# Kernel optimization log

Hardware: AMD Instinct MI355X
Metric: run time of the kernel (lower is better)

The kernel has to match this reference:

```python
import jax, jax.numpy as jnp
import numpy as np

MARGIN = 0.3  # hard-coded in all three MarginRankingLoss instances


def setup_inputs() -> dict:
    key = jax.random.key(0)
    k1, k2, k3, k4 = jax.random.split(key, 4)
    n, d, num_ids = 4096, 2048, 100
    inputs = jax.random.normal(k1, (n, d), dtype=jnp.float32)
    targets_a = jax.random.randint(k2, (n,), 0, num_ids, dtype=jnp.int64)
    targets_b = jax.random.randint(k3, (n,), 0, num_ids, dtype=jnp.int64)
    lam = jax.random.uniform(k4, (), dtype=jnp.float32)
    epoch = 60
    return {"inputs": inputs, "targets_a": targets_a, "targets_b": targets_b,
            "lam": lam, "epoch": epoch}


def reference(inputs, targets_a, targets_b, lam, epoch):
    # pairwise euclidean distance: dist[i,j] = ||x_i - x_j||
    sq = jnp.sum(inputs * inputs, axis=1)                      # [n]
    dist = sq[:, None] + sq[None, :] - 2.0 * (inputs @ inputs.T)
    dist = jnp.sqrt(jnp.clip(dist, 1e-12))                     # [n, n]

    ma = targets_a[:, None] == targets_a[None, :]
    mb = targets_b[:, None] == targets_b[None, :]
    m_same_ab = ma & mb                                        # same a AND b (incl. diagonal)
    m_same_or = (ma & ~mb) | (~ma & mb)                        # exactly one of a/b matches
    m_dif_ab = ~ma & ~mb                                       # neither matches

    ninf = -jnp.inf
    pinf = jnp.inf
    hp = jnp.max(jnp.where(m_same_ab, dist, ninf), axis=1)     # hardest positive
    hn = jnp.min(jnp.where(m_dif_ab, dist, pinf), axis=1)      # hardest negative
    max_or = jnp.max(jnp.where(m_same_or, dist, ninf), axis=1)
    min_or = jnp.min(jnp.where(m_same_or, dist, pinf), axis=1)

    use_or = m_same_or.any(axis=1) & (epoch > 50)
    sp = jnp.where(use_or, max_or, hp)
    sn = jnp.where(use_or, min_or, hn)

    # MarginRankingLoss(x1, x2, y=1) = mean(relu(x2 - x1 + margin))
    loss_1 = jnp.mean(jnp.maximum(0.0, hp - hn + MARGIN))
    loss_2 = jnp.mean(jnp.maximum(0.0, sp - hn + MARGIN))
    loss_3 = jnp.mean(jnp.maximum(0.0, hp - sn + MARGIN))
    return loss_1 + loss_2 + loss_3
```

## Files before the change

### kernel.cpp

```cpp
#include <hip/hip_runtime.h>
#include <hip/hip_bf16.h>

#define NROW 4096
#define KDIM 2048
#define ROWB (KDIM * 2)
#define BT 256
#define BK 64
#define NT (KDIM / BK)
#define LDSBUF 65536
#define PHI(r) (((r) & 7) << 4)

typedef __attribute__((ext_vector_type(8))) short bf16x8;
typedef __attribute__((ext_vector_type(4))) float f32x4;
typedef __attribute__((ext_vector_type(4))) unsigned short u16x4;

__device__ __forceinline__ unsigned short f2bf(float x) {
    unsigned u = __float_as_uint(x);
    unsigned r = (u + 0x7FFFu + ((u >> 16) & 1u)) >> 16;
    return (unsigned short)r;
}
__device__ __forceinline__ float bf2f(unsigned short b) {
    return __uint_as_float(((unsigned)b) << 16);
}

__global__ __launch_bounds__(256) void k_convert(const float* __restrict__ X,
                                                 unsigned short* __restrict__ Xb,
                                                 float* __restrict__ sqv) {
    const int row = blockIdx.x;
    const int t = threadIdx.x;
    const float4* xr = (const float4*)(X + (size_t)row * KDIM);
    unsigned short* br = Xb + (size_t)row * KDIM;
    float acc = 0.f;
#pragma unroll
    for (int it = 0; it < 2; ++it) {
        int idx = t * 2 + it;
        float4 v = xr[idx];
        u16x4 b;
        b.x = f2bf(v.x); b.y = f2bf(v.y); b.z = f2bf(v.z); b.w = f2bf(v.w);
        float f0 = bf2f(b.x), f1 = bf2f(b.y), f2 = bf2f(b.z), f3 = bf2f(b.w);
        acc += f0 * f0 + f1 * f1 + f2 * f2 + f3 * f3;
        *(u16x4*)(br + idx * 4) = b;
    }
#pragma unroll
    for (int s = 32; s > 0; s >>= 1) acc += __shfl_xor(acc, s);
    __shared__ float red[4];
    const int lane = t & 63, wid = t >> 6;
    if (lane == 0) red[wid] = acc;
    __syncthreads();
    if (t == 0) sqv[row] = red[0] + red[1] + red[2] + red[3];
}

__global__ __launch_bounds__(256) void k_init(unsigned* hp, unsigned* hn,
                                              unsigned* mor, unsigned* mir,
                                              int* anyor, float* out) {
    int i = blockIdx.x * 256 + threadIdx.x;
    hp[i] = 0u;
    hn[i] = 0x7F800000u;
    mor[i] = 0u;
    mir[i] = 0x7F800000u;
    anyor[i] = 0;
    if (i == 0) out[0] = 0.f;
}

__global__ __launch_bounds__(512, 2) void k_gemm(const unsigned short* __restrict__ Xb,
                                                 const float* __restrict__ sqv,
                                                 const int* __restrict__ ta,
                                                 const int* __restrict__ tb,
                                                 unsigned int* __restrict__ hp,
                                                 unsigned int* __restrict__ hn,
                                                 unsigned int* __restrict__ mor,
                                                 unsigned int* __restrict__ mir,
                                                 int* __restrict__ anyor) {
    __shared__ char lds[2 * LDSBUF];
    const int bi = blockIdx.x >> 4;
    const int bj = blockIdx.x & 15;
    const int t = threadIdx.x;
    const int lane = t & 63;
    const int w = t >> 6;
    const int wm = w >> 2;
    const int wn = w & 3;
    const int l15 = lane & 15;
    const int kg16 = (lane >> 4) * 16;
    const char* xbase = (const char*)Xb;

    int aoff[8][2], boff[4][2];
#pragma unroll
    for (int m = 0; m < 8; ++m) {
        const int r = wm * 128 + m * 16 + l15;
#pragma unroll
        for (int ks = 0; ks < 2; ++ks)
            aoff[m][ks] = r * 128 + ((ks * 64 + kg16) ^ PHI(r));
    }
#pragma unroll
    for (int n = 0; n < 4; ++n) {
        const int j = wn * 64 + n * 16 + l15;
#pragma unroll
        for (int ks = 0; ks < 2; ++ks)
            boff[n][ks] = 32768 + j * 128 + ((ks * 64 + kg16) ^ PHI(j));
    }

    f32x4 acc[8][4] = {};

#define STAGE(tt, p)                                                          \
    do {                                                                      \
        constexpr int isb_ = (p) >= 4;                                        \
        constexpr int c_ = (p) - isb_ * 4;                                    \
        const int row_ = c_ * 64 + (t >> 3);                                  \
        const int gr_ = (isb_ ? bj : bi) * BT + row_;                         \
        const char* gsrc_ = xbase + (size_t)gr_ * ROWB + (size_t)(tt) * 128 + \
                            (((t & 7) * 16) ^ PHI(row_));                     \
        char* ldst_ = lds + ((tt) & 1) * LDSBUF + isb_ * 32768 + row_ * 128 + \
                      (t & 7) * 16;                                           \
        __builtin_amdgcn_global_load_lds(                                     \
            (const __attribute__((address_space(1))) void*)gsrc_,             \
            (__attribute__((address_space(3))) void*)ldst_, 16, 0, 0);        \
    } while (0)

    STAGE(0, 0); STAGE(0, 2); STAGE(0, 4); STAGE(0, 5);
    STAGE(0, 6); STAGE(0, 7); STAGE(0, 1); STAGE(0, 3);
    asm volatile("s_waitcnt vmcnt(2)" ::: "memory");
    __builtin_amdgcn_s_barrier();

    bf16x8 af[4][2], bfr[4][2];
    for (int tk = 0; tk < NT; ++tk) {
        const char* bufb = lds + (tk & 1) * LDSBUF;
        const bool stg = (tk + 1) < NT;

        if (stg) { STAGE(tk + 1, 0); STAGE(tk + 1, 2); STAGE(tk + 1, 4); STAGE(tk + 1, 5); }
#pragma unroll
        for (int m = 0; m < 4; ++m) {
            af[m][0] = *(const bf16x8*)(bufb + aoff[m][0]);
            af[m][1] = *(const bf16x8*)(bufb + aoff[m][1]);
        }
#pragma unroll
        for (int n = 0; n < 2; ++n) {
            bfr[n][0] = *(const bf16x8*)(bufb + boff[n][0]);
            bfr[n][1] = *(const bf16x8*)(bufb + boff[n][1]);
        }
        __builtin_amdgcn_s_barrier();
        __builtin_amdgcn_s_setprio(1);
#pragma unroll
        for (int ks = 0; ks < 2; ++ks)
#pragma unroll
            for (int m = 0; m < 4; ++m) {
                acc[m][0] = __builtin_amdgcn_mfma_f32_16x16x32_bf16(af[m][ks], bfr[0][ks], acc[m][0], 0, 0, 0);
                acc[m][1] = __builtin_amdgcn_mfma_f32_16x16x32_bf16(af[m][ks], bfr[1][ks], acc[m][1], 0, 0, 0);
            }
        __builtin_amdgcn_s_setprio(0);
        __builtin_amdgcn_s_barrier();

        if (stg) { STAGE(tk + 1, 6); STAGE(tk + 1, 7); STAGE(tk + 1, 1); STAGE(tk + 1, 3); }
#pragma unroll
        for (int n = 2; n < 4; ++n) {
            bfr[n][0] = *(const bf16x8*)(bufb + boff[n][0]);
            bfr[n][1] = *(const bf16x8*)(bufb + boff[n][1]);
        }
        __builtin_amdgcn_s_barrier();
        __builtin_amdgcn_s_setprio(1);
#pragma unroll
        for (int ks = 0; ks < 2; ++ks)
#pragma unroll
            for (int m = 0; m < 4; ++m) {
                acc[m][2] = __builtin_amdgcn_mfma_f32_16x16x32_bf16(af[m][ks], bfr[2][ks], acc[m][2], 0, 0, 0);
                acc[m][3] = __builtin_amdgcn_mfma_f32_16x16x32_bf16(af[m][ks], bfr[3][ks], acc[m][3], 0, 0, 0);
            }
        __builtin_amdgcn_s_setprio(0);
        if (stg)
            asm volatile("s_waitcnt vmcnt(8)" ::: "memory");
        else
            asm volatile("s_waitcnt vmcnt(0)" ::: "memory");
        __builtin_amdgcn_s_barrier();

#pragma unroll
        for (int m = 0; m < 4; ++m) {
            af[m][0] = *(const bf16x8*)(bufb + aoff[4 + m][0]);
            af[m][1] = *(const bf16x8*)(bufb + aoff[4 + m][1]);
        }
        __builtin_amdgcn_s_barrier();
        __builtin_amdgcn_s_setprio(1);
#pragma unroll
        for (int ks = 0; ks < 2; ++ks)
#pragma unroll
            for (int m = 0; m < 4; ++m) {
                acc[4 + m][2] = __builtin_amdgcn_mfma_f32_16x16x32_bf16(af[m][ks], bfr[2][ks], acc[4 + m][2], 0, 0, 0);
                acc[4 + m][3] = __builtin_amdgcn_mfma_f32_16x16x32_bf16(af[m][ks], bfr[3][ks], acc[4 + m][3], 0, 0, 0);
            }
        __builtin_amdgcn_s_setprio(0);
        __builtin_amdgcn_s_barrier();

        __builtin_amdgcn_s_setprio(1);
#pragma unroll
        for (int ks = 0; ks < 2; ++ks)
#pragma unroll
            for (int m = 0; m < 4; ++m) {
                acc[4 + m][0] = __builtin_amdgcn_mfma_f32_16x16x32_bf16(af[m][ks], bfr[0][ks], acc[4 + m][0], 0, 0, 0);
                acc[4 + m][1] = __builtin_amdgcn_mfma_f32_16x16x32_bf16(af[m][ks], bfr[1][ks], acc[4 + m][1], 0, 0, 0);
            }
        __builtin_amdgcn_s_setprio(0);
        if (stg) asm volatile("s_waitcnt vmcnt(2)" ::: "memory");
        __builtin_amdgcn_s_barrier();
    }
#undef STAGE

    float sqj[4];
    int taj[4], tbj[4];
#pragma unroll
    for (int n = 0; n < 4; ++n) {
        int j = bj * BT + wn * 64 + n * 16 + l15;
        sqj[n] = sqv[j];
        taj[n] = ta[j];
        tbj[n] = tb[j];
    }
    const float INF = __uint_as_float(0x7F800000u);
#pragma unroll
    for (int m = 0; m < 8; ++m) {
#pragma unroll
        for (int reg = 0; reg < 4; ++reg) {
            const int i = bi * BT + wm * 128 + m * 16 + (lane >> 4) * 4 + reg;
            const float sqi = sqv[i];
            const int tai = ta[i], tbi = tb[i];
            float vhp = 0.f, vhn = INF, vmor = 0.f, vmir = INF, vany = 0.f;
#pragma unroll
            for (int n = 0; n < 4; ++n) {
                float d2 = sqi + sqj[n] - 2.f * acc[m][n][reg];
                float d = sqrtf(fmaxf(d2, 1e-12f));
                bool ma = (tai == taj[n]), mb = (tbi == tbj[n]);
                if (ma && mb) {
                    vhp = fmaxf(vhp, d);
                } else if (ma != mb) {
                    vmor = fmaxf(vmor, d);
                    vmir = fminf(vmir, d);
                    vany = 1.f;
                } else {
                    vhn = fminf(vhn, d);
                }
            }
#pragma unroll
            for (int s = 1; s < 16; s <<= 1) {
                vhp = fmaxf(vhp, __shfl_xor(vhp, s, 16));
                vhn = fminf(vhn, __shfl_xor(vhn, s, 16));
                vmor = fmaxf(vmor, __shfl_xor(vmor, s, 16));
                vmir = fminf(vmir, __shfl_xor(vmir, s, 16));
                vany = fmaxf(vany, __shfl_xor(vany, s, 16));
            }
            if (l15 == 0) {
                if (vhp > 0.f) atomicMax(&hp[i], __float_as_uint(vhp));
                if (vhn < INF) atomicMin(&hn[i], __float_as_uint(vhn));
                if (vany > 0.f) {
                    atomicMax(&mor[i], __float_as_uint(vmor));
                    atomicMin(&mir[i], __float_as_uint(vmir));
                    atomicOr(&anyor[i], 1);
                }
            }
        }
    }
}

__global__ __launch_bounds__(256) void k_final(const unsigned* __restrict__ hp,
                                               const unsigned* __restrict__ hn,
                                               const unsigned* __restrict__ mor,
                                               const unsigned* __restrict__ mir,
                                               const int* __restrict__ anyor,
                                               const int* __restrict__ epoch_p,
                                               float* __restrict__ out) {
    const int t = threadIdx.x;
    const int i = blockIdx.x * 256 + t;
    const bool eok = (*epoch_p > 50);
    float fhp = __uint_as_float(hp[i]);
    float fhn = __uint_as_float(hn[i]);
    bool use_or = (anyor[i] != 0) && eok;
    float sp = use_or ? __uint_as_float(mor[i]) : fhp;
    float sn = use_or ? __uint_as_float(mir[i]) : fhn;
    float s = fmaxf(0.f, fhp - fhn + 0.3f) + fmaxf(0.f, sp - fhn + 0.3f) +
              fmaxf(0.f, fhp - sn + 0.3f);
#pragma unroll
    for (int sh = 32; sh > 0; sh >>= 1) s += __shfl_xor(s, sh);
    __shared__ float red[4];
    const int lane = t & 63, wid = t >> 6;
    if (lane == 0) red[wid] = s;
    __syncthreads();
    if (t == 0)
        atomicAdd(out, (red[0] + red[1] + red[2] + red[3]) * (1.f / 4096.f));
}

extern "C" void kernel_launch(void* const* d_in, const int* in_sizes, int n_in,
                              void* d_out, int out_size, void* d_ws, size_t ws_size,
                              hipStream_t stream) {
    const float* X = (const float*)d_in[0];
    const int* ta = (const int*)d_in[1];
    const int* tb = (const int*)d_in[2];
    const int* epoch_p = (const int*)d_in[4];
    float* out = (float*)d_out;

    char* ws = (char*)d_ws;
    unsigned short* Xb = (unsigned short*)ws;
    size_t off = (size_t)NROW * KDIM * sizeof(unsigned short);
    float* sqv = (float*)(ws + off); off += (size_t)NROW * 4;
    unsigned* hp = (unsigned*)(ws + off); off += (size_t)NROW * 4;
    unsigned* hn = (unsigned*)(ws + off); off += (size_t)NROW * 4;
    unsigned* mor = (unsigned*)(ws + off); off += (size_t)NROW * 4;
    unsigned* mir = (unsigned*)(ws + off); off += (size_t)NROW * 4;
    int* anyor = (int*)(ws + off); off += (size_t)NROW * 4;

    k_convert<<<NROW, 256, 0, stream>>>(X, Xb, sqv);
    k_init<<<NROW / 256, 256, 0, stream>>>(hp, hn, mor, mir, anyor, out);
    k_gemm<<<(NROW / BT) * (NROW / BT), 512, 0, stream>>>(Xb, sqv, ta, tb,
                                                          hp, hn, mor, mir, anyor);
    k_final<<<NROW / 256, 256, 0, stream>>>(hp, hn, mor, mir, anyor, epoch_p, out);
}
```

Before: 109.6 us.

## Prefetch next tile's A/B fragments across iterations and cut barriers in GEMM loop

Restructures the main MFMA loop so the first A fragments and B01 fragments for the next k-tile are loaded from the other LDS buffer at the end of the current iteration, using separate register sets (af0/af1, b01/b23). It reorders the global-to-LDS staging so more loads are issued up front, and drops several block barriers per iteration. It also replaces the per-fragment offset arrays with two base offsets plus constant strides to free registers. The goal is to overlap LDS reads with MFMA work and reduce sync stalls, at the cost of more live fragment registers and tighter correctness constraints on the waitcnt and barrier placement for buffer reuse.

Result: no change. 108.2 us (-1.3%).

```diff
diff --git a/kernel.cpp b/kernel.cpp
--- a/kernel.cpp
+++ b/kernel.cpp
@@ -13,6 +13,8 @@
 typedef __attribute__((ext_vector_type(8))) short bf16x8;
 typedef __attribute__((ext_vector_type(4))) float f32x4;
 typedef __attribute__((ext_vector_type(4))) unsigned short u16x4;
+
+#define MFMA16(a, b, c) __builtin_amdgcn_mfma_f32_16x16x32_bf16((a), (b), (c), 0, 0, 0)
 
 __device__ __forceinline__ unsigned short f2bf(float x) {
     unsigned u = __float_as_uint(x);
@@ -83,20 +85,13 @@
     const int kg16 = (lane >> 4) * 16;
     const char* xbase = (const char*)Xb;
 
-    int aoff[8][2], boff[4][2];
-#pragma unroll
-    for (int m = 0; m < 8; ++m) {
-        const int r = wm * 128 + m * 16 + l15;
-#pragma unroll
-        for (int ks = 0; ks < 2; ++ks)
-            aoff[m][ks] = r * 128 + ((ks * 64 + kg16) ^ PHI(r));
-    }
-#pragma unroll
-    for (int n = 0; n < 4; ++n) {
-        const int j = wn * 64 + n * 16 + l15;
-#pragma unroll
-        for (int ks = 0; ks < 2; ++ks)
-            boff[n][ks] = 32768 + j * 128 + ((ks * 64 + kg16) ^ PHI(j));
+    const int P = (l15 & 7) << 4;
+    int akb[2], bkb[2];
+#pragma unroll
+    for (int ks = 0; ks < 2; ++ks) {
+        const int kx = (ks * 64 + kg16) ^ P;
+        akb[ks] = (wm * 128 + l15) * 128 + kx;
+        bkb[ks] = 32768 + (wn * 64 + l15) * 128 + kx;
     }
 
     f32x4 acc[8][4] = {};
@@ -121,83 +116,97 @@
     asm volatile("s_waitcnt vmcnt(2)" ::: "memory");
     __builtin_amdgcn_s_barrier();
 
-    bf16x8 af[4][2], bfr[4][2];
+    bf16x8 af0[4][2], af1[4][2], b01[2][2], b23[2][2];
+#pragma unroll
+    for (int ks = 0; ks < 2; ++ks) {
+#pragma unroll
+        for (int m = 0; m < 4; ++m)
+            af0[m][ks] = *(const bf16x8*)(lds + akb[ks] + m * 2048);
+        b01[0][ks] = *(const bf16x8*)(lds + bkb[ks]);
+        b01[1][ks] = *(const bf16x8*)(lds + bkb[ks] + 2048);
+    }
+
     for (int tk = 0; tk < NT; ++tk) {
-        const char* bufb = lds + (tk & 1) * LDSBUF;
+        const char* bufc = lds + (tk & 1) * LDSBUF;
+        const char* bufn = lds + ((tk + 1) & 1) * LDSBUF;
         const bool stg = (tk + 1) < NT;
 
-        if (stg) { STAGE(tk + 1, 0); STAGE(tk + 1, 2); STAGE(tk + 1, 4); STAGE(tk + 1, 5); }
-#pragma unroll
-        for (int m = 0; m < 4; ++m) {
-            af[m][0] = *(const bf16x8*)(bufb + aoff[m][0]);
-            af[m][1] = *(const bf16x8*)(bufb + aoff[m][1]);
-        }
-#pragma unroll
-        for (int n = 0; n < 2; ++n) {
-            bfr[n][0] = *(const bf16x8*)(bufb + boff[n][0]);
-            bfr[n][1] = *(const bf16x8*)(bufb + boff[n][1]);
+        if (stg) {
+            STAGE(tk + 1, 0); STAGE(tk + 1, 2); STAGE(tk + 1, 4);
+            STAGE(tk + 1, 5); STAGE(tk + 1, 6); STAGE(tk + 1, 7);
+        }
+#pragma unroll
+        for (int ks = 0; ks < 2; ++ks) {
+            b23[0][ks] = *(const bf16x8*)(bufc + bkb[ks] + 2 * 2048);
+            b23[1][ks] = *(const bf16x8*)(bufc + bkb[ks] + 3 * 2048);
+        }
+        __builtin_amdgcn_s_setprio(1);
+#pragma unroll
+        for (int ks = 0; ks < 2; ++ks)
+#pragma unroll
+            for (int m = 0; m < 4; ++m) {
+                acc[m][0] = MFMA16(af0[m][ks], b01[0][ks], acc[m][0]);
+                acc[m][1] = MFMA16(af0[m][ks], b01[1][ks], acc[m][1]);
+            }
+        __builtin_amdgcn_s_setprio(0);
+
+        if (stg) {
+            STAGE(tk + 1, 1); STAGE(tk + 1, 3);
+            asm volatile("s_waitcnt vmcnt(8)" ::: "memory");
+        } else {
+            asm volatile("s_waitcnt vmcnt(0)" ::: "memory");
         }
         __builtin_amdgcn_s_barrier();
+#pragma unroll
+        for (int ks = 0; ks < 2; ++ks)
+#pragma unroll
+            for (int m = 0; m < 4; ++m)
+                af1[m][ks] = *(const bf16x8*)(bufc + akb[ks] + (4 + m) * 2048);
         __builtin_amdgcn_s_setprio(1);
 #pragma unroll
         for (int ks = 0; ks < 2; ++ks)
 #pragma unroll
             for (int m = 0; m < 4; ++m) {
-                acc[m][0] = __builtin_amdgcn_mfma_f32_16x16x32_bf16(af[m][ks], bfr[0][ks], acc[m][0], 0, 0, 0);
-                acc[m][1] = __builtin_amdgcn_mfma_f32_16x16x32_bf16(af[m][ks], bfr[1][ks], acc[m][1], 0, 0, 0);
+                acc[m][2] = MFMA16(af0[m][ks], b23[0][ks], acc[m][2]);
+                acc[m][3] = MFMA16(af0[m][ks], b23[1][ks], acc[m][3]);
             }
         __builtin_amdgcn_s_setprio(0);
-        __builtin_amdgcn_s_barrier();
-
-        if (stg) { STAGE(tk + 1, 6); STAGE(tk + 1, 7); STAGE(tk + 1, 1); STAGE(tk + 1, 3); }
-#pragma unroll
-        for (int n = 2; n < 4; ++n) {
-            bfr[n][0] = *(const bf16x8*)(bufb + boff[n][0]);
-            bfr[n][1] = *(const bf16x8*)(bufb + boff[n][1]);
-        }
-        __builtin_amdgcn_s_barrier();
+
+        if (stg) {
+            asm volatile("s_waitcnt vmcnt(2)" ::: "memory");
+            __builtin_amdgcn_s_barrier();
+#pragma unroll
+            for (int ks = 0; ks < 2; ++ks)
+#pragma unroll
+                for (int m = 0; m < 4; ++m)
+                    af0[m][ks] = *(const bf16x8*)(bufn + akb[ks] + m * 2048);
+        }
         __builtin_amdgcn_s_setprio(1);
 #pragma unroll
         for (int ks = 0; ks < 2; ++ks)
 #pragma unroll
             for (int m = 0; m < 4; ++m) {
-                acc[m][2] = __builtin_amdgcn_mfma_f32_16x16x32_bf16(af[m][ks], bfr[2][ks], acc[m][2], 0, 0, 0);
-                acc[m][3] = __builtin_amdgcn_mfma_f32_16x16x32_bf16(af[m][ks], bfr[3][ks], acc[m][3], 0, 0, 0);
+                acc[4 + m][2] = MFMA16(af1[m][ks], b23[0][ks], acc[4 + m][2]);
+                acc[4 + m][3] = MFMA16(af1[m][ks], b23[1][ks], acc[4 + m][3]);
             }
         __builtin_amdgcn_s_setprio(0);
-        if (stg)
-            asm volatile("s_waitcnt vmcnt(8)" ::: "memory");
-        else
-            asm volatile("s_waitcnt vmcnt(0)" ::: "memory");
-        __builtin_amdgcn_s_barrier();
-
-#pragma unroll
-        for (int m = 0; m < 4; ++m) {
-            af[m][0] = *(const bf16x8*)(bufb + aoff[4 + m][0]);
-            af[m][1] = *(const bf16x8*)(bufb + aoff[4 + m][1]);
-        }
-        __builtin_amdgcn_s_barrier();
+
         __builtin_amdgcn_s_setprio(1);
 #pragma unroll
         for (int ks = 0; ks < 2; ++ks)
 #pragma unroll
             for (int m = 0; m < 4; ++m) {
-                acc[4 + m][2] = __builtin_amdgcn_mfma_f32_16x16x32_bf16(af[m][ks], bfr[2][ks], acc[4 + m][2], 0, 0, 0);
-                acc[4 + m][3] = __builtin_amdgcn_mfma_f32_16x16x32_bf16(af[m][ks], bfr[3][ks], acc[4 + m][3], 0, 0, 0);
+                acc[4 + m][0] = MFMA16(af1[m][ks], b01[0][ks], acc[4 + m][0]);
+                acc[4 + m][1] = MFMA16(af1[m][ks], b01[1][ks], acc[4 + m][1]);
             }
         __builtin_amdgcn_s_setprio(0);
-        __builtin_amdgcn_s_barrier();
-
-        __builtin_amdgcn_s_setprio(1);
-#pragma unroll
-        for (int ks = 0; ks < 2; ++ks)
-#pragma unroll
-            for (int m = 0; m < 4; ++m) {
-                acc[4 + m][0] = __builtin_amdgcn_mfma_f32_16x16x32_bf16(af[m][ks], bfr[0][ks], acc[4 + m][0], 0, 0, 0);
-                acc[4 + m][1] = __builtin_amdgcn_mfma_f32_16x16x32_bf16(af[m][ks], bfr[1][ks], acc[4 + m][1], 0, 0, 0);
-            }
-        __builtin_amdgcn_s_setprio(0);
-        if (stg) asm volatile("s_waitcnt vmcnt(2)" ::: "memory");
+        if (stg) {
+#pragma unroll
+            for (int ks = 0; ks < 2; ++ks) {
+                b01[0][ks] = *(const bf16x8*)(bufn + bkb[ks]);
+                b01[1][ks] = *(const bf16x8*)(bufn + bkb[ks] + 2048);
+            }
+        }
         __builtin_amdgcn_s_barrier();
     }
 #undef STAGE
```
